# Performance work log

Hardware: AMD Instinct MI355X
Metric: run time of the kernel (lower is better)

The kernel has to match this reference:

```python
import jax, jax.numpy as jnp
import numpy as np

B = 16384
D = 1024          # in_features
R = 64            # low_rank
E = 4             # num_experts
L = 3             # layer_num


def setup_inputs() -> dict:
    key = jax.random.key(0)
    ks = jax.random.split(key, 6)
    # xavier-normal-ish scales
    s_uv = (2.0 / (D + R)) ** 0.5
    s_c = (2.0 / (R + R)) ** 0.5
    s_g = (2.0 / (D + 1)) ** 0.5
    return {
        "inputs": jax.random.normal(ks[0], (B, D), dtype=jnp.float32),
        "U": jax.random.normal(ks[1], (L, E, D, R), dtype=jnp.float32) * s_uv,
        "V": jax.random.normal(ks[2], (L, E, D, R), dtype=jnp.float32) * s_uv,
        "C": jax.random.normal(ks[3], (L, E, R, R), dtype=jnp.float32) * s_c,
        "gate_w": jax.random.normal(ks[4], (E, D), dtype=jnp.float32) * s_g,
        "bias": jnp.zeros((L, D), dtype=jnp.float32),
    }


def reference(inputs, U, V, C, gate_w, bias):
    x0 = inputs                                  # [B, D]
    x_l = x0
    for i in range(L):
        # gating: per-expert Linear(d,1) on x_l -> [B, E], softmax over experts
        gates = jax.nn.softmax(x_l @ gate_w.T, axis=1)        # [B, E]
        # v_x = tanh(V_e^T x_l) for all experts at once
        v = jnp.tanh(jnp.einsum('bd,edr->ber', x_l, V[i]))    # [B, E, R]
        v = jnp.tanh(jnp.einsum('ers,bes->ber', C[i], v))     # [B, E, R]
        uv = jnp.einsum('edr,ber->bed', U[i], v)              # [B, E, D]
        dot = x0[:, None, :] * (uv + bias[i][None, None, :])  # [B, E, D]
        moe_out = jnp.einsum('bed,be->bd', dot, gates)        # [B, D]
        x_l = moe_out + x_l
    return x_l
```

## Files before the change

kernel.cpp:

```cpp
#include <hip/hip_runtime.h>
#include <math.h>

#define BB 16384
#define DD 1024
#define RR 64
#define EE 4
#define ER 256
#define LL 3

#define LDM 72

typedef __bf16 bf16x8 __attribute__((ext_vector_type(8)));
typedef float f32x4 __attribute__((ext_vector_type(4)));
typedef unsigned short us;

static __device__ inline us f2b(float f) {
    union { float f; unsigned u; } c; c.f = f;
    return (us)((c.u + 0x7FFF + ((c.u >> 16) & 1)) >> 16);
}
static __device__ inline float b2f(us v) {
    union { unsigned u; float f; } c; c.u = ((unsigned)v) << 16;
    return c.f;
}
static __device__ inline float fast_tanh(float x) {
    float t = __expf(2.f * x);
    return 1.f - 2.f / (t + 1.f);
}
static __device__ __forceinline__ void ld_lds16(const us* g, us* l) {
    __builtin_amdgcn_global_load_lds((const __attribute__((address_space(1))) void*)g,
                                     (__attribute__((address_space(3))) void*)l, 16, 0, 0);
}

__global__ __launch_bounds__(256) void convF2B(const float* __restrict__ s, us* __restrict__ d) {
    int f = (blockIdx.x * 256 + threadIdx.x) * 4;
    float4 v = *(const float4*)&s[f];
    *(ushort4*)&d[f] = make_ushort4(f2b(v.x), f2b(v.y), f2b(v.z), f2b(v.w));
}
__global__ __launch_bounds__(256) void convV(const float* __restrict__ V, us* __restrict__ Vt) {
    const int le = blockIdx.x;
    const int d0 = blockIdx.y * 64;
    __shared__ float t[64 * 65];
    const int tid = threadIdx.x;
    const float* Vb = V + (size_t)le * DD * RR;
    #pragma unroll
    for (int p = 0; p < 4; ++p) {
        int f = tid + p * 256; int dd = f >> 4; int c = (f & 15) * 4;
        float4 v = *(const float4*)&Vb[(size_t)(d0 + dd) * RR + c];
        t[dd * 65 + c + 0] = v.x; t[dd * 65 + c + 1] = v.y;
        t[dd * 65 + c + 2] = v.z; t[dd * 65 + c + 3] = v.w;
    }
    __syncthreads();
    int r = tid >> 2, dg = (tid & 3) * 16;
    us o[16];
    #pragma unroll
    for (int k = 0; k < 16; ++k) o[k] = f2b(t[(dg + k) * 65 + r]);
    us* dst = Vt + (size_t)le * RR * DD + (size_t)r * DD + d0 + dg;
    #pragma unroll
    for (int q = 0; q < 4; ++q) *(ushort4*)&dst[q * 4] = *(ushort4*)&o[q * 4];
}

__global__ __launch_bounds__(512, 2) void gemm1_fused(const us* __restrict__ xs,
                                                      const us* __restrict__ Vt,
                                                      const us* __restrict__ Ce,
                                                      const us* __restrict__ gwb,
                                                      us* __restrict__ w) {
    const int row0 = blockIdx.x * 64;
    const int tid = threadIdx.x;
    const int lane = tid & 63, wave = tid >> 6;
    const int l15 = lane & 15, quad = lane >> 4;
    const int e = wave & 3, h = wave >> 2;
    const int e64 = e * 64;

    __shared__ __align__(16) union {
        struct { us buf[4][10240]; us gw[4096]; float gates[256]; } s;
        us Tt[4][64 * LDM];
    } u;

    const int kcA  = (lane & 3) ^ ((lane >> 3) & 3);
    const int sA   = quad ^ ((l15 >> 1) & 3);
    const int rsub = lane >> 2;

    ld_lds16(gwb + (size_t)(lane & 3) * DD + (wave * 16 + rsub) * 8, &u.s.gw[wave * 512]);

    auto STAGE = [&](int bi, int k0) {
        us* bb = u.s.buf[bi];
        #pragma unroll
        for (int j = 0; j < 2; ++j) {
            int row = wave * 32 + j * 16 + rsub;
            ld_lds16(Vt + (size_t)row * DD + k0 + kcA * 8, &bb[(wave * 32 + j * 16) * 32]);
        }
        if (wave < 4) {
            int row = wave * 16 + rsub;
            ld_lds16(xs + (size_t)(row0 + row) * DD + k0 + kcA * 8, &bb[8192 + wave * 512]);
        }
    };

    f32x4 acc[4][2] = {};
    f32x4 accg = {};
    STAGE(0, 0); STAGE(1, 32); STAGE(2, 64);

    for (int t = 0; t < 32; ++t) {
        if (t < 30) {
            if (wave < 4) asm volatile("s_waitcnt vmcnt(6)" ::: "memory");
            else          asm volatile("s_waitcnt vmcnt(4)" ::: "memory");
        } else if (t == 30) {
            if (wave < 4) asm volatile("s_waitcnt vmcnt(3)" ::: "memory");
            else          asm volatile("s_waitcnt vmcnt(2)" ::: "memory");
        } else {
            asm volatile("s_waitcnt vmcnt(0)" ::: "memory");
        }
        __builtin_amdgcn_s_barrier();
        if (t < 29) STAGE((t + 3) & 3, (t + 3) * 32);
        __builtin_amdgcn_sched_barrier(0);
        const us* bb = u.s.buf[t & 3];
        bf16x8 af[4], bfr[2];
        #pragma unroll
        for (int mt = 0; mt < 4; ++mt)
            af[mt] = *(const bf16x8*)&bb[(e64 + mt * 16 + l15) * 32 + sA * 8];
        #pragma unroll
        for (int nt = 0; nt < 2; ++nt)
            bfr[nt] = *(const bf16x8*)&bb[8192 + (h * 32 + nt * 16 + l15) * 32 + sA * 8];
        #pragma unroll
        for (int mt = 0; mt < 4; ++mt)
            #pragma unroll
            for (int nt = 0; nt < 2; ++nt)
                acc[mt][nt] = __builtin_amdgcn_mfma_f32_16x16x32_bf16(af[mt], bfr[nt], acc[mt][nt], 0, 0, 0);
        if (wave < 4) {
            bf16x8 bfrg = *(const bf16x8*)&bb[8192 + (wave * 16 + l15) * 32 + sA * 8];
            bf16x8 afg  = *(const bf16x8*)&u.s.gw[(t * 4 + quad) * 32 + (l15 & 3) * 8];
            accg = __builtin_amdgcn_mfma_f32_16x16x32_bf16(afg, bfrg, accg, 0, 0, 0);
        }
    }
    __builtin_amdgcn_s_barrier();
    __builtin_amdgcn_sched_barrier(0);

    us* Tt = u.Tt[e];
    #pragma unroll
    for (int mt = 0; mt < 4; ++mt)
        #pragma unroll
        for (int nt = 0; nt < 2; ++nt) {
            int b = h * 32 + nt * 16 + l15;
            us o[4];
            #pragma unroll
            for (int i = 0; i < 4; ++i) o[i] = f2b(fast_tanh(acc[mt][nt][i]));
            *(ushort4*)&Tt[b * LDM + mt * 16 + quad * 4] = *(ushort4*)o;
        }
    if (wave < 4 && quad == 0) {
        float l0 = accg[0], l1 = accg[1], l2 = accg[2], l3 = accg[3];
        float m = fmaxf(fmaxf(l0, l1), fmaxf(l2, l3));
        float g0 = __expf(l0 - m), g1 = __expf(l1 - m);
        float g2 = __expf(l2 - m), g3 = __expf(l3 - m);
        float inv = 1.f / (g0 + g1 + g2 + g3);
        int b = wave * 16 + l15;
        u.s.gates[0 * 64 + b] = g0 * inv; u.s.gates[1 * 64 + b] = g1 * inv;
        u.s.gates[2 * 64 + b] = g2 * inv; u.s.gates[3 * 64 + b] = g3 * inv;
    }
    __syncthreads();

    const us* Cb = Ce + (size_t)e * RR * RR;
    f32x4 acc2[4][2] = {};
    #pragma unroll
    for (int ks = 0; ks < 2; ++ks) {
        bf16x8 af2[4], bf2[2];
        #pragma unroll
        for (int mt = 0; mt < 4; ++mt)
            af2[mt] = *(const bf16x8*)&Cb[(size_t)(mt * 16 + l15) * RR + ks * 32 + quad * 8];
        #pragma unroll
        for (int nt = 0; nt < 2; ++nt)
            bf2[nt] = *(const bf16x8*)&Tt[(h * 32 + nt * 16 + l15) * LDM + ks * 32 + quad * 8];
        #pragma unroll
        for (int mt = 0; mt < 4; ++mt)
            #pragma unroll
            for (int nt = 0; nt < 2; ++nt)
                acc2[mt][nt] = __builtin_amdgcn_mfma_f32_16x16x32_bf16(af2[mt], bf2[nt], acc2[mt][nt], 0, 0, 0);
    }
    #pragma unroll
    for (int mt = 0; mt < 4; ++mt)
        #pragma unroll
        for (int nt = 0; nt < 2; ++nt) {
            int b = h * 32 + nt * 16 + l15;
            float g = u.s.gates[e64 + b];
            us o[4];
            #pragma unroll
            for (int i = 0; i < 4; ++i) o[i] = f2b(g * fast_tanh(acc2[mt][nt][i]));
            *(ushort4*)&w[(size_t)(row0 + b) * ER + e64 + mt * 16 + quad * 4] = *(ushort4*)o;
        }
}

__global__ __launch_bounds__(512, 4) void gemm2_combine(const us* __restrict__ w,
                                                        const us* __restrict__ Ub,
                                                        const us* __restrict__ x0b,
                                                        const us* __restrict__ xls,
                                                        us* __restrict__ xbo,
                                                        const float* __restrict__ biasl,
                                                        float* __restrict__ out, int last) {
    const int row0 = blockIdx.x * 128;
    const int d0 = blockIdx.y * 128;
    __shared__ __align__(16) union { us stage[2][8192]; float smf[8192]; } su;
    const int tid = threadIdx.x;
    const int lane = tid & 63, wave = tid >> 6;
    const int bh = wave & 1, dh = wave >> 1;
    const int l15 = lane & 15, quad = lane >> 4;

    const int kcA = (lane & 3) ^ ((lane >> 3) & 3);
    const int sA  = quad ^ ((l15 >> 1) & 3);

    auto STAGE = [&](int bi, int s) {
        int e = s >> 1, r0q = (s & 1) * 32;
        us* bb = su.stage[bi];
        int row = wave * 16 + (lane >> 2);
        ld_lds16(Ub + ((size_t)e * DD + d0 + row) * RR + r0q + kcA * 8, &bb[wave * 512]);
        ld_lds16(w + (size_t)(row0 + row) * ER + e * 64 + r0q + kcA * 8, &bb[4096 + wave * 512]);
    };

    f32x4 acc[2][4] = {};
    STAGE(0, 0);
    for (int t = 0; t < 8; ++t) {
        __builtin_amdgcn_s_barrier();
        if (t < 7) {
            STAGE((t + 1) & 1, t + 1);
            asm volatile("s_waitcnt vmcnt(2)" ::: "memory");
        } else {
            asm volatile("s_waitcnt vmcnt(0)" ::: "memory");
        }
        __builtin_amdgcn_s_barrier();
        __builtin_amdgcn_sched_barrier(0);
        const us* bb = su.stage[t & 1];
        bf16x8 af[2], bfr[4];
        #pragma unroll
        for (int mt = 0; mt < 2; ++mt)
            af[mt] = *(const bf16x8*)&bb[(dh * 32 + mt * 16 + l15) * 32 + sA * 8];
        #pragma unroll
        for (int nt = 0; nt < 4; ++nt)
            bfr[nt] = *(const bf16x8*)&bb[4096 + (bh * 64 + nt * 16 + l15) * 32 + sA * 8];
        #pragma unroll
        for (int mt = 0; mt < 2; ++mt)
            #pragma unroll
            for (int nt = 0; nt < 4; ++nt)
                acc[mt][nt] = __builtin_amdgcn_mfma_f32_16x16x32_bf16(af[mt], bfr[nt], acc[mt][nt], 0, 0, 0);
    }

    const int erow = tid >> 2;
    const int ec   = tid & 3;
    const size_t gb = (size_t)(row0 + erow) * DD + d0;
    #pragma unroll
    for (int p = 0; p < 2; ++p) {
        const int doff = p * 64 + ec * 16;
        uint xu[8], lu[8];
        *(uint4*)&xu[0] = *(const uint4*)&x0b[gb + doff];
        *(uint4*)&xu[4] = *(const uint4*)&x0b[gb + doff + 8];
        *(uint4*)&lu[0] = *(const uint4*)&xls[gb + doff];
        *(uint4*)&lu[4] = *(const uint4*)&xls[gb + doff + 8];
        float bf[16];
        *(float4*)&bf[0]  = *(const float4*)&biasl[d0 + doff];
        *(float4*)&bf[4]  = *(const float4*)&biasl[d0 + doff + 4];
        *(float4*)&bf[8]  = *(const float4*)&biasl[d0 + doff + 8];
        *(float4*)&bf[12] = *(const float4*)&biasl[d0 + doff + 12];
        __syncthreads();
        if ((dh >> 1) == p) {
            #pragma unroll
            for (int mt = 0; mt < 2; ++mt)
                #pragma unroll
                for (int nt = 0; nt < 4; ++nt) {
                    int r = bh * 64 + nt * 16 + l15;
                    int s = (dh & 1) * 8 + mt * 4 + quad;
                    *(f32x4*)&su.smf[r * 64 + ((s ^ (r & 15)) << 2)] = acc[mt][nt];
                }
        }
        __syncthreads();
        float o[16];
        #pragma unroll
        for (int j = 0; j < 4; ++j) {
            int s = ec * 4 + j;
            float4 a = *(const float4*)&su.smf[erow * 64 + ((s ^ (erow & 15)) << 2)];
            #pragma unroll
            for (int i = 0; i < 4; ++i) {
                int k = j * 4 + i;
                float av = (i == 0) ? a.x : (i == 1) ? a.y : (i == 2) ? a.z : a.w;
                uint uu = xu[k >> 1], ll = lu[k >> 1];
                float xv = b2f((k & 1) ? (us)(uu >> 16) : (us)(uu & 0xffff));
                float xl = b2f((k & 1) ? (us)(ll >> 16) : (us)(ll & 0xffff));
                o[k] = xv * (av + bf[k]) + xl;
            }
        }
        if (last) {
            *(float4*)&out[gb + doff]      = *(float4*)&o[0];
            *(float4*)&out[gb + doff + 4]  = *(float4*)&o[4];
            *(float4*)&out[gb + doff + 8]  = *(float4*)&o[8];
            *(float4*)&out[gb + doff + 12] = *(float4*)&o[12];
        } else {
            us ob[16];
            #pragma unroll
            for (int k = 0; k < 16; ++k) ob[k] = f2b(o[k]);
            *(uint4*)&xbo[gb + doff]     = *(uint4*)&ob[0];
            *(uint4*)&xbo[gb + doff + 8] = *(uint4*)&ob[8];
        }
    }
}

extern "C" void kernel_launch(void* const* d_in, const int* in_sizes, int n_in,
                              void* d_out, int out_size, void* d_ws, size_t ws_size,
                              hipStream_t stream) {
    const float* inputs = (const float*)d_in[0];
    const float* U      = (const float*)d_in[1];
    const float* V      = (const float*)d_in[2];
    const float* C      = (const float*)d_in[3];
    const float* gw     = (const float*)d_in[4];
    const float* bias   = (const float*)d_in[5];
    float* out = (float*)d_out;

    us* xb0 = (us*)d_ws;
    us* xb  = xb0 + (size_t)BB * DD;
    us* wbf = xb + (size_t)BB * DD;
    us* gwb = wbf + (size_t)BB * ER;
    us* Vt  = gwb + (size_t)EE * DD;
    us* Ub  = Vt + (size_t)LL * EE * RR * DD;
    us* Cb  = Ub + (size_t)LL * EE * DD * RR;

    convF2B<<<dim3(BB * DD / 1024), 256, 0, stream>>>(inputs, xb0);
    convF2B<<<dim3(LL * EE * DD * RR / 1024), 256, 0, stream>>>(U, Ub);
    convF2B<<<dim3(LL * EE * RR * RR / 1024), 256, 0, stream>>>(C, Cb);
    convF2B<<<dim3(EE * DD / 1024), 256, 0, stream>>>(gw, gwb);
    convV<<<dim3(LL * EE, DD / 64), 256, 0, stream>>>(V, Vt);

    for (int i = 0; i < LL; ++i) {
        const us* xs = (i == 0) ? xb0 : xb;
        gemm1_fused<<<dim3(BB / 64), 512, 0, stream>>>(
            xs, Vt + (size_t)i * EE * RR * DD, Cb + (size_t)i * EE * RR * RR, gwb, wbf);
        gemm2_combine<<<dim3(BB / 128, DD / 128), 512, 0, stream>>>(
            wbf, Ub + (size_t)i * EE * DD * RR, xb0, xs, xb, bias + (size_t)i * DD,
            out, i == LL - 1);
    }
}
```

Measured before the change: 279.1 us.

## Fuse the low-rank GEMMs and the combine into one per-layer kernel

The two per-layer kernels become one. The gated low-rank activations w are kept in swizzled LDS instead of being written to and read back from a global workspace, and each 64-row block then computes the U projection across all of D. The combine epilogue goes through a per-wave LDS scratch. This removes one launch per layer and the global round trip of w. In exchange, every block now reads the whole U matrix for the layer straight from global/L2 with no LDS staging, and only 256 blocks do the output stage instead of 1024.

```diff
diff --git a/kernel.cpp b/kernel.cpp
--- a/kernel.cpp
+++ b/kernel.cpp
@@ -59,11 +59,15 @@
     for (int q = 0; q < 4; ++q) *(ushort4*)&dst[q * 4] = *(ushort4*)&o[q * 4];
 }
 
-__global__ __launch_bounds__(512, 2) void gemm1_fused(const us* __restrict__ xs,
+__global__ __launch_bounds__(512, 2) void layer_fused(const us* __restrict__ xs,
                                                       const us* __restrict__ Vt,
                                                       const us* __restrict__ Ce,
                                                       const us* __restrict__ gwb,
-                                                      us* __restrict__ w) {
+                                                      const us* __restrict__ x0b,
+                                                      const us* __restrict__ Ub,
+                                                      us* __restrict__ xbo,
+                                                      const float* __restrict__ biasl,
+                                                      float* __restrict__ out, int last) {
     const int row0 = blockIdx.x * 64;
     const int tid = threadIdx.x;
     const int lane = tid & 63, wave = tid >> 6;
@@ -74,6 +78,7 @@
     __shared__ __align__(16) union {
         struct { us buf[4][10240]; us gw[4096]; float gates[256]; } s;
         us Tt[4][64 * LDM];
+        struct { us wlds[64 * 256]; float smf[8][1024]; } p2;
     } u;
 
     const int kcA  = (lane & 3) ^ ((lane >> 3) & 3);
@@ -134,17 +139,19 @@
     __builtin_amdgcn_s_barrier();
     __builtin_amdgcn_sched_barrier(0);
 
-    us* Tt = u.Tt[e];
-    #pragma unroll
-    for (int mt = 0; mt < 4; ++mt)
-        #pragma unroll
-        for (int nt = 0; nt < 2; ++nt) {
-            int b = h * 32 + nt * 16 + l15;
-            us o[4];
-            #pragma unroll
-            for (int i = 0; i < 4; ++i) o[i] = f2b(fast_tanh(acc[mt][nt][i]));
-            *(ushort4*)&Tt[b * LDM + mt * 16 + quad * 4] = *(ushort4*)o;
-        }
+    {
+        us* Tt = u.Tt[e];
+        #pragma unroll
+        for (int mt = 0; mt < 4; ++mt)
+            #pragma unroll
+            for (int nt = 0; nt < 2; ++nt) {
+                int b = h * 32 + nt * 16 + l15;
+                us o[4];
+                #pragma unroll
+                for (int i = 0; i < 4; ++i) o[i] = f2b(fast_tanh(acc[mt][nt][i]));
+                *(ushort4*)&Tt[b * LDM + mt * 16 + quad * 4] = *(ushort4*)o;
+            }
+    }
     if (wave < 4 && quad == 0) {
         float l0 = accg[0], l1 = accg[1], l2 = accg[2], l3 = accg[3];
         float m = fmaxf(fmaxf(l0, l1), fmaxf(l2, l3));
@@ -167,13 +174,15 @@
             af2[mt] = *(const bf16x8*)&Cb[(size_t)(mt * 16 + l15) * RR + ks * 32 + quad * 8];
         #pragma unroll
         for (int nt = 0; nt < 2; ++nt)
-            bf2[nt] = *(const bf16x8*)&Tt[(h * 32 + nt * 16 + l15) * LDM + ks * 32 + quad * 8];
+            bf2[nt] = *(const bf16x8*)&u.Tt[e][(h * 32 + nt * 16 + l15) * LDM + ks * 32 + quad * 8];
         #pragma unroll
         for (int mt = 0; mt < 4; ++mt)
             #pragma unroll
             for (int nt = 0; nt < 2; ++nt)
                 acc2[mt][nt] = __builtin_amdgcn_mfma_f32_16x16x32_bf16(af2[mt], bf2[nt], acc2[mt][nt], 0, 0, 0);
     }
+    __syncthreads();
+
     #pragma unroll
     for (int mt = 0; mt < 4; ++mt)
         #pragma unroll
@@ -183,117 +192,90 @@
             us o[4];
             #pragma unroll
             for (int i = 0; i < 4; ++i) o[i] = f2b(g * fast_tanh(acc2[mt][nt][i]));
-            *(ushort4*)&w[(size_t)(row0 + b) * ER + e64 + mt * 16 + quad * 4] = *(ushort4*)o;
-        }
-}
-
-__global__ __launch_bounds__(512, 4) void gemm2_combine(const us* __restrict__ w,
-                                                        const us* __restrict__ Ub,
-                                                        const us* __restrict__ x0b,
-                                                        const us* __restrict__ xls,
-                                                        us* __restrict__ xbo,
-                                                        const float* __restrict__ biasl,
-                                                        float* __restrict__ out, int last) {
-    const int row0 = blockIdx.x * 128;
-    const int d0 = blockIdx.y * 128;
-    __shared__ __align__(16) union { us stage[2][8192]; float smf[8192]; } su;
-    const int tid = threadIdx.x;
-    const int lane = tid & 63, wave = tid >> 6;
-    const int bh = wave & 1, dh = wave >> 1;
-    const int l15 = lane & 15, quad = lane >> 4;
-
-    const int kcA = (lane & 3) ^ ((lane >> 3) & 3);
-    const int sA  = quad ^ ((l15 >> 1) & 3);
-
-    auto STAGE = [&](int bi, int s) {
-        int e = s >> 1, r0q = (s & 1) * 32;
-        us* bb = su.stage[bi];
-        int row = wave * 16 + (lane >> 2);
-        ld_lds16(Ub + ((size_t)e * DD + d0 + row) * RR + r0q + kcA * 8, &bb[wave * 512]);
-        ld_lds16(w + (size_t)(row0 + row) * ER + e * 64 + r0q + kcA * 8, &bb[4096 + wave * 512]);
-    };
-
-    f32x4 acc[2][4] = {};
-    STAGE(0, 0);
-    for (int t = 0; t < 8; ++t) {
-        __builtin_amdgcn_s_barrier();
-        if (t < 7) {
-            STAGE((t + 1) & 1, t + 1);
-            asm volatile("s_waitcnt vmcnt(2)" ::: "memory");
-        } else {
-            asm volatile("s_waitcnt vmcnt(0)" ::: "memory");
-        }
-        __builtin_amdgcn_s_barrier();
-        __builtin_amdgcn_sched_barrier(0);
-        const us* bb = su.stage[t & 1];
-        bf16x8 af[2], bfr[4];
-        #pragma unroll
-        for (int mt = 0; mt < 2; ++mt)
-            af[mt] = *(const bf16x8*)&bb[(dh * 32 + mt * 16 + l15) * 32 + sA * 8];
-        #pragma unroll
-        for (int nt = 0; nt < 4; ++nt)
-            bfr[nt] = *(const bf16x8*)&bb[4096 + (bh * 64 + nt * 16 + l15) * 32 + sA * 8];
-        #pragma unroll
-        for (int mt = 0; mt < 2; ++mt)
-            #pragma unroll
-            for (int nt = 0; nt < 4; ++nt)
-                acc[mt][nt] = __builtin_amdgcn_mfma_f32_16x16x32_bf16(af[mt], bfr[nt], acc[mt][nt], 0, 0, 0);
-    }
-
-    const int erow = tid >> 2;
-    const int ec   = tid & 3;
-    const size_t gb = (size_t)(row0 + erow) * DD + d0;
-    #pragma unroll
+            int col = e64 + mt * 16 + quad * 4;
+            int cc = col >> 3, off = col & 7;
+            *(ushort4*)&u.p2.wlds[b * 256 + ((cc ^ (b & 7)) << 3) + off] = *(ushort4*)o;
+        }
+    __syncthreads();
+
+    const int bl = lane >> 2, dc3 = lane & 3;
+    #pragma unroll 1
     for (int p = 0; p < 2; ++p) {
-        const int doff = p * 64 + ec * 16;
-        uint xu[8], lu[8];
-        *(uint4*)&xu[0] = *(const uint4*)&x0b[gb + doff];
-        *(uint4*)&xu[4] = *(const uint4*)&x0b[gb + doff + 8];
-        *(uint4*)&lu[0] = *(const uint4*)&xls[gb + doff];
-        *(uint4*)&lu[4] = *(const uint4*)&xls[gb + doff + 8];
-        float bf[16];
-        *(float4*)&bf[0]  = *(const float4*)&biasl[d0 + doff];
-        *(float4*)&bf[4]  = *(const float4*)&biasl[d0 + doff + 4];
-        *(float4*)&bf[8]  = *(const float4*)&biasl[d0 + doff + 8];
-        *(float4*)&bf[12] = *(const float4*)&biasl[d0 + doff + 12];
-        __syncthreads();
-        if ((dh >> 1) == p) {
-            #pragma unroll
-            for (int mt = 0; mt < 2; ++mt)
+        const int dw = p * 512 + wave * 64;
+        f32x4 pac[4][4] = {};
+        #pragma unroll
+        for (int s = 0; s < 8; ++s) {
+            int e2 = s >> 1, r0 = (s & 1) * 32;
+            bf16x8 af[4], bfr[4];
+            #pragma unroll
+            for (int mt = 0; mt < 4; ++mt) {
+                int d = dw + mt * 16 + l15;
+                af[mt] = *(const bf16x8*)&Ub[((size_t)e2 * DD + d) * RR + r0 + quad * 8];
+            }
+            #pragma unroll
+            for (int nt = 0; nt < 4; ++nt) {
+                int b = nt * 16 + l15;
+                int cc = e2 * 8 + (r0 >> 3) + quad;
+                bfr[nt] = *(const bf16x8*)&u.p2.wlds[b * 256 + ((cc ^ (b & 7)) << 3)];
+            }
+            #pragma unroll
+            for (int mt = 0; mt < 4; ++mt)
                 #pragma unroll
-                for (int nt = 0; nt < 4; ++nt) {
-                    int r = bh * 64 + nt * 16 + l15;
-                    int s = (dh & 1) * 8 + mt * 4 + quad;
-                    *(f32x4*)&su.smf[r * 64 + ((s ^ (r & 15)) << 2)] = acc[mt][nt];
+                for (int nt = 0; nt < 4; ++nt)
+                    pac[mt][nt] = __builtin_amdgcn_mfma_f32_16x16x32_bf16(af[mt], bfr[nt], pac[mt][nt], 0, 0, 0);
+        }
+        const int dg = dw + dc3 * 16;
+        float bfv[16];
+        *(float4*)&bfv[0]  = *(const float4*)&biasl[dg];
+        *(float4*)&bfv[4]  = *(const float4*)&biasl[dg + 4];
+        *(float4*)&bfv[8]  = *(const float4*)&biasl[dg + 8];
+        *(float4*)&bfv[12] = *(const float4*)&biasl[dg + 12];
+        float* smf = u.p2.smf[wave];
+        #pragma unroll
+        for (int nt = 0; nt < 4; ++nt) {
+            #pragma unroll
+            for (int mt = 0; mt < 4; ++mt) {
+                int ch = (mt * 4 + quad) ^ (l15 & 7);
+                *(f32x4*)&smf[l15 * 64 + ch * 4] = pac[mt][nt];
+            }
+            asm volatile("s_waitcnt lgkmcnt(0)" ::: "memory");
+            __builtin_amdgcn_sched_barrier(0);
+            const int brow = row0 + nt * 16 + bl;
+            const size_t gb = (size_t)brow * DD + dg;
+            uint xu[8], lu[8];
+            *(uint4*)&xu[0] = *(const uint4*)&x0b[gb];
+            *(uint4*)&xu[4] = *(const uint4*)&x0b[gb + 8];
+            *(uint4*)&lu[0] = *(const uint4*)&xs[gb];
+            *(uint4*)&lu[4] = *(const uint4*)&xs[gb + 8];
+            float o[16];
+            #pragma unroll
+            for (int j = 0; j < 4; ++j) {
+                int ch = (dc3 * 4 + j) ^ (bl & 7);
+                float4 a = *(const float4*)&smf[bl * 64 + ch * 4];
+                #pragma unroll
+                for (int i = 0; i < 4; ++i) {
+                    int k = j * 4 + i;
+                    float av = (i == 0) ? a.x : (i == 1) ? a.y : (i == 2) ? a.z : a.w;
+                    uint uu = xu[k >> 1], ll = lu[k >> 1];
+                    float xv = b2f((k & 1) ? (us)(uu >> 16) : (us)(uu & 0xffff));
+                    float xl = b2f((k & 1) ? (us)(ll >> 16) : (us)(ll & 0xffff));
+                    o[k] = xv * (av + bfv[k]) + xl;
                 }
-        }
-        __syncthreads();
-        float o[16];
-        #pragma unroll
-        for (int j = 0; j < 4; ++j) {
-            int s = ec * 4 + j;
-            float4 a = *(const float4*)&su.smf[erow * 64 + ((s ^ (erow & 15)) << 2)];
-            #pragma unroll
-            for (int i = 0; i < 4; ++i) {
-                int k = j * 4 + i;
-                float av = (i == 0) ? a.x : (i == 1) ? a.y : (i == 2) ? a.z : a.w;
-                uint uu = xu[k >> 1], ll = lu[k >> 1];
-                float xv = b2f((k & 1) ? (us)(uu >> 16) : (us)(uu & 0xffff));
-                float xl = b2f((k & 1) ? (us)(ll >> 16) : (us)(ll & 0xffff));
-                o[k] = xv * (av + bf[k]) + xl;
-            }
-        }
-        if (last) {
-            *(float4*)&out[gb + doff]      = *(float4*)&o[0];
-            *(float4*)&out[gb + doff + 4]  = *(float4*)&o[4];
-            *(float4*)&out[gb + doff + 8]  = *(float4*)&o[8];
-            *(float4*)&out[gb + doff + 12] = *(float4*)&o[12];
-        } else {
-            us ob[16];
-            #pragma unroll
-            for (int k = 0; k < 16; ++k) ob[k] = f2b(o[k]);
-            *(uint4*)&xbo[gb + doff]     = *(uint4*)&ob[0];
-            *(uint4*)&xbo[gb + doff + 8] = *(uint4*)&ob[8];
+            }
+            if (last) {
+                *(float4*)&out[gb]      = *(float4*)&o[0];
+                *(float4*)&out[gb + 4]  = *(float4*)&o[4];
+                *(float4*)&out[gb + 8]  = *(float4*)&o[8];
+                *(float4*)&out[gb + 12] = *(float4*)&o[12];
+            } else {
+                us ob[16];
+                #pragma unroll
+                for (int k = 0; k < 16; ++k) ob[k] = f2b(o[k]);
+                *(uint4*)&xbo[gb]     = *(uint4*)&ob[0];
+                *(uint4*)&xbo[gb + 8] = *(uint4*)&ob[8];
+            }
+            asm volatile("s_waitcnt lgkmcnt(0)" ::: "memory");
+            __builtin_amdgcn_sched_barrier(0);
         }
     }
 }
@@ -311,8 +293,7 @@
 
     us* xb0 = (us*)d_ws;
     us* xb  = xb0 + (size_t)BB * DD;
-    us* wbf = xb + (size_t)BB * DD;
-    us* gwb = wbf + (size_t)BB * ER;
+    us* gwb = xb + (size_t)BB * DD;
     us* Vt  = gwb + (size_t)EE * DD;
     us* Ub  = Vt + (size_t)LL * EE * RR * DD;
     us* Cb  = Ub + (size_t)LL * EE * DD * RR;
@@ -325,10 +306,9 @@
 
     for (int i = 0; i < LL; ++i) {
         const us* xs = (i == 0) ? xb0 : xb;
-        gemm1_fused<<<dim3(BB / 64), 512, 0, stream>>>(
-            xs, Vt + (size_t)i * EE * RR * DD, Cb + (size_t)i * EE * RR * RR, gwb, wbf);
-        gemm2_combine<<<dim3(BB / 128, DD / 128), 512, 0, stream>>>(
-            wbf, Ub + (size_t)i * EE * DD * RR, xb0, xs, xb, bias + (size_t)i * DD,
+        layer_fused<<<dim3(BB / 64), 512, 0, stream>>>(
+            xs, Vt + (size_t)i * EE * RR * DD, Cb + (size_t)i * EE * RR * RR, gwb,
+            xb0, Ub + (size_t)i * EE * DD * RR, xb, bias + (size_t)i * DD,
             out, i == LL - 1);
     }
 }
```

New measurement: 278.7 us. Within noise of the previous version (-0.1%).
